# Optimization experiments

Hardware: AMD Instinct MI355X
Metric: run time of the kernel (lower is better)

## Reference

```python
import jax, jax.numpy as jnp
import numpy as np

NH, NKV, HD, H = 32, 8, 128, 4096
G = NH // NKV  # GQA group size = 4
EPS = 1e-5
SCALE = HD ** -0.5


def rms_norm(x, w, eps=EPS):
    # per-head RMSNorm over last dim, computed in fp32
    xf = x.astype(jnp.float32)
    var = jnp.mean(xf * xf, axis=-1, keepdims=True)
    return (w * (xf * jax.lax.rsqrt(var + eps)).astype(x.dtype))


def setup_inputs() -> dict:
    key = jax.random.key(0)
    ks = jax.random.split(key, 4)
    B, SQ, SKV = 4, 1024, 1601
    return {
        "hidden_states": jax.random.normal(ks[0], (B, SQ, H), jnp.float32),
        "cross_attention_states": jax.random.normal(ks[1], (B, SKV, H), jnp.float32),
        "wqkv": jax.random.normal(ks[2], ((NH + 2 * NKV) * HD, H), jnp.float32) * 0.02,
        "wo": jax.random.normal(ks[3], (NH * HD, H), jnp.float32) * 0.02,
        "q_norm_weight": jnp.ones((HD,), jnp.float32),
        "k_norm_weight": jnp.ones((HD,), jnp.float32),
    }


def reference(hidden_states, cross_attention_states, wqkv, wo, q_norm_weight, k_norm_weight):
    B, SQ, _ = hidden_states.shape
    SKV = cross_attention_states.shape[1]
    q_sz, kv_sz = NH * HD, NKV * HD

    # fused QKV projection on decoder tokens -> keep only q
    qkv_dec = jnp.einsum('bsh,oh->bso', hidden_states, wqkv)
    q = qkv_dec[..., :q_sz]
    # fused QKV projection on encoder tokens -> keep only k, v
    qkv_enc = jnp.einsum('bsh,oh->bso', cross_attention_states, wqkv)
    k = qkv_enc[..., q_sz:q_sz + kv_sz]
    v = qkv_enc[..., q_sz + kv_sz:]

    q = rms_norm(q.reshape(B, SQ, NH, HD), q_norm_weight)      # [B,SQ,NH,HD]
    k = rms_norm(k.reshape(B, SKV, NKV, HD), k_norm_weight)    # [B,SKV,NKV,HD]
    v = v.reshape(B, SKV, NKV, HD)

    # GQA: group query heads per kv head
    qg = q.reshape(B, SQ, NKV, G, HD)
    scores = jnp.einsum('bqkgd,bskd->bkgqs', qg, k) * SCALE    # [B,NKV,G,SQ,SKV]
    probs = jax.nn.softmax(scores, axis=-1)
    out = jnp.einsum('bkgqs,bskd->bqkgd', probs, v)            # [B,SQ,NKV,G,HD]
    out = out.reshape(B, SQ, NH * HD)
    return jnp.einsum('bso,ho->bsh', out, wo.T.T) if False else jnp.einsum('bsf,hf->bsh', out, wo)
```

## Files before the change

kernel.cpp:

```cpp
#include <hip/hip_runtime.h>
#include <cstdint>
#include <math.h>

typedef _Float16 f16;
typedef __attribute__((ext_vector_type(4))) _Float16 f16x4;
typedef __attribute__((ext_vector_type(8))) _Float16 f16x8;
typedef __attribute__((ext_vector_type(4))) float f32x4;

__device__ inline void gload_lds16(const void* g, void* l) {
  auto gp = reinterpret_cast<const __attribute__((address_space(1))) uint32_t*>(
      reinterpret_cast<uintptr_t>(g));
  auto lp = reinterpret_cast<__attribute__((address_space(3))) uint32_t*>(
      reinterpret_cast<uintptr_t>(l));
  __builtin_amdgcn_global_load_lds(gp, lp, 16 , 0, 0);
}

__global__ __launch_bounds__(256) void cvtzero_kernel(const float* __restrict__ s0, f16* __restrict__ d0,
                                                      const float* __restrict__ s1, f16* __restrict__ d1,
                                                      const float* __restrict__ s2, f16* __restrict__ d2,
                                                      float4* __restrict__ z) {
  int idx = blockIdx.x * blockDim.x + threadIdx.x;
  int stride = gridDim.x * blockDim.x;
  for (int i = idx; i < 18747392; i += stride) {
    const float* src; f16* dst; int k;
    if (i < 4194304) { src = s0; dst = d0; k = i; }
    else if (i < 10752000) { src = s1; dst = d1; k = i - 4194304; }
    else if (i < 17043456) { src = s2; dst = d2; k = i - 10752000; }
    else { float4 zr = {0.f, 0.f, 0.f, 0.f}; z[i - 17043456] = zr; continue; }
    float4 v = reinterpret_cast<const float4*>(src)[k];
    f16x4 h;
    h.x = (f16)v.x; h.y = (f16)v.y; h.z = (f16)v.z; h.w = (f16)v.w;
    reinterpret_cast<f16x4*>(dst)[k] = h;
  }
}

__global__ __launch_bounds__(256) void cvt_kernel(const float* __restrict__ src,
                                                  f16* __restrict__ dst, int n4) {
  int idx = blockIdx.x * blockDim.x + threadIdx.x;
  int stride = gridDim.x * blockDim.x;
  for (int i = idx; i < n4; i += stride) {
    float4 v = reinterpret_cast<const float4*>(src)[i];
    f16x4 h;
    h.x = (f16)v.x; h.y = (f16)v.y; h.z = (f16)v.z; h.w = (f16)v.w;
    reinterpret_cast<f16x4*>(dst)[i] = h;
  }
}

template <bool MB, int EPI>
__global__ __launch_bounds__(512, 2) void gemm256(const f16* __restrict__ A,
                                                  const f16* __restrict__ Bw,
                                                  float* __restrict__ C,
                                                  f16* __restrict__ Ch,
                                                  const float* __restrict__ wvec,
                                                  f16* __restrict__ Vtf,
                                                  int M, int N, int K) {
  __shared__ f16 As[2][256][64];
  __shared__ f16 Bs[2][256][64];
  const int tid = threadIdx.x;
  const int l = tid & 63, w = tid >> 6;
  const int lq = l & 15, lk = l >> 4;
  const int wm = w >> 2, wn = w & 3;
  const int nwg = gridDim.x * gridDim.y;
  const int p = blockIdx.y * gridDim.x + blockIdx.x;
  const int L = (p & 7) * (nwg >> 3) + (p >> 3);
  const int bx = L % gridDim.x, by = L / gridDim.x;
  const int brow = by * 256, bcol = bx * 256;
  const int KT = K >> 6;

  const int srow8 = w * 8 + (l >> 3);
  const int scol  = ((l & 7) ^ (l >> 3)) * 8;
  const int swz   = (lq & 7) << 4;

  f32x4 acc[8][4];
  f32x4 zf = {0.f, 0.f, 0.f, 0.f};
#pragma unroll
  for (int m = 0; m < 8; ++m)
#pragma unroll
    for (int n = 0; n < 4; ++n) acc[m][n] = zf;

  auto stageA = [&](int kt, int buf, int i) {
    int ra = brow + i * 64 + srow8;
    if (MB) ra = (ra < M) ? ra : (M - 1);
    gload_lds16(A + (size_t)ra * K + kt * 64 + scol,
                (char*)(&As[buf][0][0]) + i * 8192 + w * 1024);
  };
  auto stageB = [&](int kt, int buf, int i) {
    int rb = bcol + i * 64 + srow8;
    gload_lds16(Bw + (size_t)rb * K + kt * 64 + scol,
                (char*)(&Bs[buf][0][0]) + i * 8192 + w * 1024);
  };
  auto ldA = [&](int buf, int m, int kk) -> f16x8 {
    int r = wm * 128 + m * 16 + lq;
    return *reinterpret_cast<const f16x8*>(
        (char*)(&As[buf][0][0]) + r * 128 + ((kk * 64 + lk * 16) ^ swz));
  };
  auto ldB = [&](int buf, int n, int kk) -> f16x8 {
    int r = wn * 64 + n * 16 + lq;
    return *reinterpret_cast<const f16x8*>(
        (char*)(&Bs[buf][0][0]) + r * 128 + ((kk * 64 + lk * 16) ^ swz));
  };

#pragma unroll
  for (int i = 0; i < 4; ++i) stageA(0, 0, i);
#pragma unroll
  for (int i = 0; i < 4; ++i) stageB(0, 0, i);

  f16x8 avA[4][2], avB[4][2], bvA[2][2], bvB[2][2];
  for (int t = 0; t < KT; ++t) {
    const int buf = t & 1, nbuf = buf ^ 1;
    const bool pf = (t + 1 < KT);

    if (pf) {
      stageA(t + 1, nbuf, 0); stageA(t + 1, nbuf, 1);
      asm volatile("s_waitcnt vmcnt(2)" ::: "memory");
    } else {
      asm volatile("s_waitcnt vmcnt(0)" ::: "memory");
    }
    __builtin_amdgcn_s_barrier();

#pragma unroll
    for (int mm = 0; mm < 4; ++mm)
#pragma unroll
      for (int kk = 0; kk < 2; ++kk) avA[mm][kk] = ldA(buf, mm, kk);
#pragma unroll
    for (int nn = 0; nn < 2; ++nn)
#pragma unroll
      for (int kk = 0; kk < 2; ++kk) bvA[nn][kk] = ldB(buf, nn, kk);
    __builtin_amdgcn_s_setprio(1);
#pragma unroll
    for (int mm = 0; mm < 4; ++mm)
#pragma unroll
      for (int nn = 0; nn < 2; ++nn)
#pragma unroll
        for (int kk = 0; kk < 2; ++kk)
          acc[mm][nn] = __builtin_amdgcn_mfma_f32_16x16x32_f16(avA[mm][kk], bvA[nn][kk], acc[mm][nn], 0, 0, 0);
    __builtin_amdgcn_s_setprio(0);
#pragma unroll
    for (int mm = 0; mm < 4; ++mm)
#pragma unroll
      for (int kk = 0; kk < 2; ++kk) avB[mm][kk] = ldA(buf, 4 + mm, kk);
    if (pf) { stageA(t + 1, nbuf, 2); stageA(t + 1, nbuf, 3); }
    asm volatile("" ::: "memory");
    __builtin_amdgcn_s_barrier();

    __builtin_amdgcn_s_setprio(1);
#pragma unroll
    for (int mm = 0; mm < 4; ++mm)
#pragma unroll
      for (int nn = 0; nn < 2; ++nn)
#pragma unroll
        for (int kk = 0; kk < 2; ++kk)
          acc[4 + mm][nn] = __builtin_amdgcn_mfma_f32_16x16x32_f16(avB[mm][kk], bvA[nn][kk], acc[4 + mm][nn], 0, 0, 0);
    __builtin_amdgcn_s_setprio(0);
#pragma unroll
    for (int nn = 0; nn < 2; ++nn)
#pragma unroll
      for (int kk = 0; kk < 2; ++kk) bvB[nn][kk] = ldB(buf, 2 + nn, kk);
    if (pf) { stageB(t + 1, nbuf, 0); stageB(t + 1, nbuf, 1); }
    asm volatile("" ::: "memory");
    __builtin_amdgcn_s_barrier();

    __builtin_amdgcn_s_setprio(1);
#pragma unroll
    for (int mm = 0; mm < 4; ++mm)
#pragma unroll
      for (int nn = 0; nn < 2; ++nn)
#pragma unroll
        for (int kk = 0; kk < 2; ++kk)
          acc[4 + mm][2 + nn] = __builtin_amdgcn_mfma_f32_16x16x32_f16(avB[mm][kk], bvB[nn][kk], acc[4 + mm][2 + nn], 0, 0, 0);
    __builtin_amdgcn_s_setprio(0);
#pragma unroll
    for (int mm = 0; mm < 4; ++mm)
#pragma unroll
      for (int kk = 0; kk < 2; ++kk) avA[mm][kk] = ldA(buf, mm, kk);
    if (pf) { stageB(t + 1, nbuf, 2); stageB(t + 1, nbuf, 3); }
    asm volatile("" ::: "memory");
    __builtin_amdgcn_s_barrier();

    __builtin_amdgcn_s_setprio(1);
#pragma unroll
    for (int mm = 0; mm < 4; ++mm)
#pragma unroll
      for (int nn = 0; nn < 2; ++nn)
#pragma unroll
        for (int kk = 0; kk < 2; ++kk)
          acc[mm][2 + nn] = __builtin_amdgcn_mfma_f32_16x16x32_f16(avA[mm][kk], bvB[nn][kk], acc[mm][2 + nn], 0, 0, 0);
    __builtin_amdgcn_s_setprio(0);
  }

  if (EPI == 0) {
#pragma unroll
    for (int m = 0; m < 8; ++m) {
#pragma unroll
      for (int j = 0; j < 4; ++j) {
        int row = brow + wm * 128 + m * 16 + lk * 4 + j;
        if (MB && row >= M) continue;
        float* dst = C + (size_t)row * N + bcol + wn * 64 + lq;
#pragma unroll
        for (int n = 0; n < 4; ++n) dst[n * 16] = acc[m][n][j];
      }
    }
  } else if (EPI == 1) {
    __shared__ float ssq[256][4];
#pragma unroll
    for (int m = 0; m < 8; ++m)
#pragma unroll
      for (int j = 0; j < 4; ++j) {
        int lr = wm * 128 + m * 16 + lk * 4 + j;
        float pp = 0.f;
#pragma unroll
        for (int n = 0; n < 4; ++n) pp += acc[m][n][j] * acc[m][n][j];
        pp += __shfl_xor(pp, 1);
        pp += __shfl_xor(pp, 2);
        pp += __shfl_xor(pp, 4);
        pp += __shfl_xor(pp, 8);
        if (lq == 0) ssq[lr][wn] = pp;
      }
    asm volatile("" ::: "memory");
    __builtin_amdgcn_s_barrier();
    const int hh = wn >> 1;
    float wv[4];
#pragma unroll
    for (int n = 0; n < 4; ++n) wv[n] = wvec[(wn * 64 + n * 16 + lq) & 127];
#pragma unroll
    for (int m = 0; m < 8; ++m)
#pragma unroll
      for (int j = 0; j < 4; ++j) {
        int lr = wm * 128 + m * 16 + lk * 4 + j;
        float ss = ssq[lr][hh * 2] + ssq[lr][hh * 2 + 1];
        float rs = rsqrtf(ss * (1.0f / 128.0f) + 1e-5f) *
                   (0.08838834764831845f * 1.4426950408889634f);
        f16* dst = Ch + (size_t)(brow + lr) * N + bcol + wn * 64 + lq;
#pragma unroll
        for (int n = 0; n < 4; ++n) dst[n * 16] = (f16)(acc[m][n][j] * rs * wv[n]);
      }
  } else {
    const bool isK = (bcol < 1024);
    __shared__ float ssq[256][4];
    if (isK) {
#pragma unroll
      for (int m = 0; m < 8; ++m)
#pragma unroll
        for (int j = 0; j < 4; ++j) {
          int lr = wm * 128 + m * 16 + lk * 4 + j;
          float pp = 0.f;
#pragma unroll
          for (int n = 0; n < 4; ++n) pp += acc[m][n][j] * acc[m][n][j];
          pp += __shfl_xor(pp, 1);
          pp += __shfl_xor(pp, 2);
          pp += __shfl_xor(pp, 4);
          pp += __shfl_xor(pp, 8);
          if (lq == 0) ssq[lr][wn] = pp;
        }
      asm volatile("" ::: "memory");
      __builtin_amdgcn_s_barrier();
    }
    const int hh = wn >> 1;
    float wv[4];
    if (isK) {
#pragma unroll
      for (int n = 0; n < 4; ++n) wv[n] = wvec[(wn * 64 + n * 16 + lq) & 127];
    }
#pragma unroll
    for (int m = 0; m < 8; ++m) {
#pragma unroll
      for (int j = 0; j < 4; ++j) {
        int lr = wm * 128 + m * 16 + lk * 4 + j;
        int r = brow + lr;
        if (r >= M) continue;
        unsigned bb = (unsigned)r / 1601u;
        unsigned s = (unsigned)r - bb * 1601u;
        if (isK) {
          float ss = ssq[lr][hh * 2] + ssq[lr][hh * 2 + 1];
          float rs = rsqrtf(ss * (1.0f / 128.0f) + 1e-5f);
#pragma unroll
          for (int n = 0; n < 4; ++n) {
            int col = wn * 64 + n * 16 + lq;
            int kvh = (bcol + col) >> 7;
            int d = col & 127;
            Ch[((size_t)(bb * 8 + kvh) * 1664 + s) * 128 + d] =
                (f16)(acc[m][n][j] * rs * wv[n]);
          }
        } else {
#pragma unroll
          for (int n = 0; n < 4; ++n) {
            int col = bcol - 1024 + wn * 64 + n * 16 + lq;
            int kvh = col >> 7;
            int d = col & 127;
            Vtf[((size_t)(bb * 8 + kvh) * 128 + d) * 1664 + s] = (f16)acc[m][n][j];
          }
        }
      }
    }
  }
}

__global__ __launch_bounds__(256, 2) void attn_kernel(const f16* __restrict__ Qf,
                                                      const f16* __restrict__ Kf,
                                                      const f16* __restrict__ Vtf,
                                                      f16* __restrict__ Oa) {
  __shared__ f16 Ksm[2][64][128];
  __shared__ f16 Vsm[2][128][64];
  __shared__ f16 Psm[4][32][64];
  const int p = blockIdx.x;
  const int L = (p & 7) * 128 + (p >> 3);
  const int qt = L & 7, h = (L >> 3) & 31, b = L >> 8;
  const int kvh = h >> 2;
  const int tid = threadIdx.x;
  const int l = tid & 63, w = tid >> 6;
  const int lq = l & 15, lk = l >> 4;

  f16x8 qreg[2][4];
  const f16* Qbase = Qf + ((size_t)(b * 1024 + qt * 128 + w * 32)) * 4096 + h * 128;
#pragma unroll
  for (int qm = 0; qm < 2; ++qm)
#pragma unroll
    for (int ks = 0; ks < 4; ++ks)
      qreg[qm][ks] = *reinterpret_cast<const f16x8*>(
          Qbase + (size_t)(qm * 16 + lq) * 4096 + ks * 32 + lk * 8);

  const f16* Kb = Kf + (size_t)(b * 8 + kvh) * (1664 * 128);
  const f16* Vb = Vtf + (size_t)(b * 8 + kvh) * (128 * 1664);

  f32x4 o[2][8];
  f32x4 zf = {0.f, 0.f, 0.f, 0.f};
  f32x4 neg8 = {-8.f, -8.f, -8.f, -8.f};
#pragma unroll
  for (int qm = 0; qm < 2; ++qm)
#pragma unroll
    for (int dn = 0; dn < 8; ++dn) o[qm][dn] = zf;
  float lrow[2][4];
#pragma unroll
  for (int qm = 0; qm < 2; ++qm)
#pragma unroll
    for (int j = 0; j < 4; ++j) lrow[qm][j] = 0.f;

  char* Pw = (char*)(&Psm[w][0][0]);
  const int swzR = (lq & 7) << 4;

  auto stageK = [&](int t, int buf) {
#pragma unroll
    for (int i = 0; i < 4; ++i) {
      int row = w * 16 + i * 4 + lk;
      int cb = (lq * 16) ^ ((row & 7) << 4);
      gload_lds16(Kb + (size_t)(t * 64 + row) * 128 + (cb >> 1),
                  (char*)(&Ksm[buf][0][0]) + w * 4096 + i * 1024);
    }
  };
  auto stageV = [&](int t, int buf) {
#pragma unroll
    for (int i = 0; i < 4; ++i) {
      int r = w * 32 + i * 8 + (l >> 3);
      int cb = ((l & 7) * 16) ^ ((r & 7) << 4);
      gload_lds16(Vb + (size_t)r * 1664 + t * 64 + (cb >> 1),
                  (char*)(&Vsm[buf][0][0]) + w * 4096 + i * 1024);
    }
  };

  stageK(0, 0);
  stageV(0, 0);
  int cur = 0;
  for (int t = 0; t < 26; ++t) {
    if (t < 25) {
      stageK(t + 1, cur ^ 1);
      stageV(t + 1, cur ^ 1);
      asm volatile("s_waitcnt vmcnt(8)" ::: "memory");
    } else {
      asm volatile("s_waitcnt vmcnt(0)" ::: "memory");
    }
    __builtin_amdgcn_s_barrier();

    f32x4 s[2][4];
#pragma unroll
    for (int qm = 0; qm < 2; ++qm)
#pragma unroll
      for (int kn = 0; kn < 4; ++kn) s[qm][kn] = neg8;
    __builtin_amdgcn_s_setprio(1);
#pragma unroll
    for (int ks = 0; ks < 4; ++ks) {
      f16x8 bf[4];
#pragma unroll
      for (int kn = 0; kn < 4; ++kn)
        bf[kn] = *reinterpret_cast<const f16x8*>(
            (char*)(&Ksm[cur][0][0]) + (kn * 16 + lq) * 256 + ((ks * 64 + lk * 16) ^ swzR));
#pragma unroll
      for (int qm = 0; qm < 2; ++qm)
#pragma unroll
        for (int kn = 0; kn < 4; ++kn)
          s[qm][kn] = __builtin_amdgcn_mfma_f32_16x16x32_f16(qreg[qm][ks], bf[kn], s[qm][kn], 0, 0, 0);
    }
    __builtin_amdgcn_s_setprio(0);

    if (t == 25) {
#pragma unroll
      for (int kn = 0; kn < 4; ++kn) {
        bool valid = (kn * 16 + lq) < 1;
#pragma unroll
        for (int qm = 0; qm < 2; ++qm)
#pragma unroll
          for (int j = 0; j < 4; ++j) s[qm][kn][j] = valid ? s[qm][kn][j] : -1e30f;
      }
    }

#pragma unroll
    for (int qm = 0; qm < 2; ++qm) {
#pragma unroll
      for (int j = 0; j < 4; ++j) {
        float rsum = 0.f;
#pragma unroll
        for (int kn = 0; kn < 4; ++kn) {
          float pv = exp2f(s[qm][kn][j]);
          s[qm][kn][j] = pv;
          rsum += pv;
        }
        lrow[qm][j] += rsum;
        int prow = qm * 16 + lk * 4 + j;
        int swzW = lk << 5;
#pragma unroll
        for (int kn = 0; kn < 4; ++kn)
          *reinterpret_cast<f16*>(Pw + prow * 128 + (((kn * 16 + lq) * 2) ^ swzW)) =
              (f16)s[qm][kn][j];
      }
    }

    __builtin_amdgcn_s_setprio(1);
#pragma unroll
    for (int c = 0; c < 2; ++c) {
      f16x8 pa[2];
#pragma unroll
      for (int qm = 0; qm < 2; ++qm) {
        int prow = qm * 16 + lq;
        pa[qm] = *reinterpret_cast<const f16x8*>(
            Pw + prow * 128 + ((c * 64 + lk * 16) ^ (((lq >> 2) & 3) << 5)));
      }
      f16x8 vb[8];
#pragma unroll
      for (int dn = 0; dn < 8; ++dn)
        vb[dn] = *reinterpret_cast<const f16x8*>(
            (char*)(&Vsm[cur][0][0]) + (dn * 16 + lq) * 128 + ((c * 64 + lk * 16) ^ swzR));
#pragma unroll
      for (int qm = 0; qm < 2; ++qm)
#pragma unroll
        for (int dn = 0; dn < 8; ++dn)
          o[qm][dn] = __builtin_amdgcn_mfma_f32_16x16x32_f16(pa[qm], vb[dn], o[qm][dn], 0, 0, 0);
    }
    __builtin_amdgcn_s_setprio(0);
    __builtin_amdgcn_s_barrier();
    cur ^= 1;
  }

#pragma unroll
  for (int qm = 0; qm < 2; ++qm) {
#pragma unroll
    for (int j = 0; j < 4; ++j) {
      float fl = lrow[qm][j];
      fl += __shfl_xor(fl, 1);
      fl += __shfl_xor(fl, 2);
      fl += __shfl_xor(fl, 4);
      fl += __shfl_xor(fl, 8);
      float il = 1.0f / fl;
      int token = b * 1024 + qt * 128 + w * 32 + qm * 16 + lk * 4 + j;
      f16* dst = Oa + (size_t)token * 4096 + h * 128;
#pragma unroll
      for (int dn = 0; dn < 8; ++dn) dst[dn * 16 + lq] = (f16)(o[qm][dn][j] * il);
    }
  }
}

extern "C" void kernel_launch(void* const* d_in, const int* in_sizes, int n_in,
                              void* d_out, int out_size, void* d_ws, size_t ws_size,
                              hipStream_t stream) {
  const float* hidden = (const float*)d_in[0];
  const float* cross  = (const float*)d_in[1];
  const float* wqkv   = (const float*)d_in[2];
  const float* wo     = (const float*)d_in[3];
  const float* qw     = (const float*)d_in[4];
  const float* kw     = (const float*)d_in[5];

  char* ws = (char*)d_ws;
  f16* hidden_h = (f16*)(ws + 0);
  f16* attn_h   = hidden_h;
  f16* wqkv_h = (f16*)(ws + 33554432);
  f16* cross_h = (f16*)(ws + 83886080);
  f16* wo_h    = (f16*)(ws + 83886080);
  f16* k_h  = (f16*)(ws + 136347648);
  f16* vt_h = (f16*)(ws + 136347648 + 13631488);
  f16* q_h = (f16*)d_out;

  cvtzero_kernel<<<2048, 256, 0, stream>>>(hidden, hidden_h, cross, cross_h,
                                           wqkv, wqkv_h, (float4*)(ws + 136347648));
  gemm256<true, 2><<<dim3(8, 26), 512, 0, stream>>>(
      cross_h, wqkv_h + (size_t)4096 * 4096, nullptr, k_h, kw, vt_h, 6404, 2048, 4096);
  cvt_kernel<<<2048, 256, 0, stream>>>(wo, wo_h, 16777216 / 4);
  gemm256<false, 1><<<dim3(16, 16), 512, 0, stream>>>(
      hidden_h, wqkv_h, nullptr, q_h, qw, nullptr, 4096, 4096, 4096);
  attn_kernel<<<1024, 256, 0, stream>>>(q_h, k_h, vt_h, attn_h);
  gemm256<false, 0><<<dim3(16, 16), 512, 0, stream>>>(
      attn_h, wo_h, (float*)d_out, nullptr, nullptr, nullptr, 4096, 4096, 4096);
}
```

Before: 605.7 us.

## Single-buffer attention K/V tiles for occupancy and fuse wo conversion into cvtzero

The attention kernel drops double-buffered K/V LDS tiles and uses single buffers. The next K tile is loaded after the QK step and the next V tile after the PV step, with launch bounds raised to allow three blocks per CU. This trades explicit prefetch overlap for more resident waves and adds extra waits and barriers per iteration. Separately, the wo fp32->fp16 conversion moves into the combined cvtzero kernel when the workspace is large enough, saving one launch but making the first kernel longer.

Result: slower. 675.0 us (+11.4%).

```diff
diff --git a/kernel.cpp b/kernel.cpp
--- a/kernel.cpp
+++ b/kernel.cpp
@@ -18,15 +18,20 @@
 __global__ __launch_bounds__(256) void cvtzero_kernel(const float* __restrict__ s0, f16* __restrict__ d0,
                                                       const float* __restrict__ s1, f16* __restrict__ d1,
                                                       const float* __restrict__ s2, f16* __restrict__ d2,
+                                                      const float* __restrict__ s3, f16* __restrict__ d3,
+                                                      int nwo,
                                                       float4* __restrict__ z) {
   int idx = blockIdx.x * blockDim.x + threadIdx.x;
   int stride = gridDim.x * blockDim.x;
-  for (int i = idx; i < 18747392; i += stride) {
+  const int nz0 = 17043456 + nwo;
+  const int total = nz0 + 1703936;
+  for (int i = idx; i < total; i += stride) {
     const float* src; f16* dst; int k;
     if (i < 4194304) { src = s0; dst = d0; k = i; }
     else if (i < 10752000) { src = s1; dst = d1; k = i - 4194304; }
     else if (i < 17043456) { src = s2; dst = d2; k = i - 10752000; }
-    else { float4 zr = {0.f, 0.f, 0.f, 0.f}; z[i - 17043456] = zr; continue; }
+    else if (i < nz0) { src = s3; dst = d3; k = i - 17043456; }
+    else { float4 zr = {0.f, 0.f, 0.f, 0.f}; z[i - nz0] = zr; continue; }
     float4 v = reinterpret_cast<const float4*>(src)[k];
     f16x4 h;
     h.x = (f16)v.x; h.y = (f16)v.y; h.z = (f16)v.z; h.w = (f16)v.w;
@@ -295,12 +300,12 @@
   }
 }
 
-__global__ __launch_bounds__(256, 2) void attn_kernel(const f16* __restrict__ Qf,
+__global__ __launch_bounds__(256, 3) void attn_kernel(const f16* __restrict__ Qf,
                                                       const f16* __restrict__ Kf,
                                                       const f16* __restrict__ Vtf,
                                                       f16* __restrict__ Oa) {
-  __shared__ f16 Ksm[2][64][128];
-  __shared__ f16 Vsm[2][128][64];
+  __shared__ f16 Ksm[64][128];
+  __shared__ f16 Vsm[128][64];
   __shared__ f16 Psm[4][32][64];
   const int p = blockIdx.x;
   const int L = (p & 7) * 128 + (p >> 3);
@@ -338,38 +343,31 @@
   char* Pw = (char*)(&Psm[w][0][0]);
   const int swzR = (lq & 7) << 4;
 
-  auto stageK = [&](int t, int buf) {
+  auto stageK = [&](int t) {
 #pragma unroll
     for (int i = 0; i < 4; ++i) {
       int row = w * 16 + i * 4 + lk;
       int cb = (lq * 16) ^ ((row & 7) << 4);
       gload_lds16(Kb + (size_t)(t * 64 + row) * 128 + (cb >> 1),
-                  (char*)(&Ksm[buf][0][0]) + w * 4096 + i * 1024);
+                  (char*)(&Ksm[0][0]) + w * 4096 + i * 1024);
     }
   };
-  auto stageV = [&](int t, int buf) {
+  auto stageV = [&](int t) {
 #pragma unroll
     for (int i = 0; i < 4; ++i) {
       int r = w * 32 + i * 8 + (l >> 3);
       int cb = ((l & 7) * 16) ^ ((r & 7) << 4);
       gload_lds16(Vb + (size_t)r * 1664 + t * 64 + (cb >> 1),
-                  (char*)(&Vsm[buf][0][0]) + w * 4096 + i * 1024);
+                  (char*)(&Vsm[0][0]) + w * 4096 + i * 1024);
     }
   };
 
-  stageK(0, 0);
-  stageV(0, 0);
-  int cur = 0;
+  stageK(0);
+  stageV(0);
+  asm volatile("s_waitcnt vmcnt(0)" ::: "memory");
+  __builtin_amdgcn_s_barrier();
+
   for (int t = 0; t < 26; ++t) {
-    if (t < 25) {
-      stageK(t + 1, cur ^ 1);
-      stageV(t + 1, cur ^ 1);
-      asm volatile("s_waitcnt vmcnt(8)" ::: "memory");
-    } else {
-      asm volatile("s_waitcnt vmcnt(0)" ::: "memory");
-    }
-    __builtin_amdgcn_s_barrier();
-
     f32x4 s[2][4];
 #pragma unroll
     for (int qm = 0; qm < 2; ++qm)
@@ -382,7 +380,7 @@
 #pragma unroll
       for (int kn = 0; kn < 4; ++kn)
         bf[kn] = *reinterpret_cast<const f16x8*>(
-            (char*)(&Ksm[cur][0][0]) + (kn * 16 + lq) * 256 + ((ks * 64 + lk * 16) ^ swzR));
+            (char*)(&Ksm[0][0]) + (kn * 16 + lq) * 256 + ((ks * 64 + lk * 16) ^ swzR));
 #pragma unroll
       for (int qm = 0; qm < 2; ++qm)
 #pragma unroll
@@ -390,6 +388,10 @@
           s[qm][kn] = __builtin_amdgcn_mfma_f32_16x16x32_f16(qreg[qm][ks], bf[kn], s[qm][kn], 0, 0, 0);
     }
     __builtin_amdgcn_s_setprio(0);
+
+    asm volatile("s_waitcnt vmcnt(0)" ::: "memory");
+    __builtin_amdgcn_s_barrier();
+    if (t < 25) stageK(t + 1);
 
     if (t == 25) {
 #pragma unroll
@@ -437,7 +439,7 @@
 #pragma unroll
       for (int dn = 0; dn < 8; ++dn)
         vb[dn] = *reinterpret_cast<const f16x8*>(
-            (char*)(&Vsm[cur][0][0]) + (dn * 16 + lq) * 128 + ((c * 64 + lk * 16) ^ swzR));
+            (char*)(&Vsm[0][0]) + (dn * 16 + lq) * 128 + ((c * 64 + lk * 16) ^ swzR));
 #pragma unroll
       for (int qm = 0; qm < 2; ++qm)
 #pragma unroll
@@ -445,8 +447,10 @@
           o[qm][dn] = __builtin_amdgcn_mfma_f32_16x16x32_f16(pa[qm], vb[dn], o[qm][dn], 0, 0, 0);
     }
     __builtin_amdgcn_s_setprio(0);
-    __builtin_amdgcn_s_barrier();
-    cur ^= 1;
+
+    asm volatile("s_waitcnt vmcnt(0)" ::: "memory");
+    __builtin_amdgcn_s_barrier();
+    if (t < 25) stageV(t + 1);
   }
 
 #pragma unroll
@@ -482,16 +486,21 @@
   f16* attn_h   = hidden_h;
   f16* wqkv_h = (f16*)(ws + 33554432);
   f16* cross_h = (f16*)(ws + 83886080);
-  f16* wo_h    = (f16*)(ws + 83886080);
   f16* k_h  = (f16*)(ws + 136347648);
   f16* vt_h = (f16*)(ws + 136347648 + 13631488);
   f16* q_h = (f16*)d_out;
 
+  const bool fuse_wo = (ws_size >= (size_t)197165056);
+  f16* wo_h = fuse_wo ? (f16*)(ws + 163610624) : (f16*)(ws + 83886080);
+
   cvtzero_kernel<<<2048, 256, 0, stream>>>(hidden, hidden_h, cross, cross_h,
-                                           wqkv, wqkv_h, (float4*)(ws + 136347648));
+                                           wqkv, wqkv_h, wo, wo_h,
+                                           fuse_wo ? 4194304 : 0,
+                                           (float4*)(ws + 136347648));
   gemm256<true, 2><<<dim3(8, 26), 512, 0, stream>>>(
       cross_h, wqkv_h + (size_t)4096 * 4096, nullptr, k_h, kw, vt_h, 6404, 2048, 4096);
-  cvt_kernel<<<2048, 256, 0, stream>>>(wo, wo_h, 16777216 / 4);
+  if (!fuse_wo)
+    cvt_kernel<<<2048, 256, 0, stream>>>(wo, wo_h, 16777216 / 4);
   gemm256<false, 1><<<dim3(16, 16), 512, 0, stream>>>(
       hidden_h, wqkv_h, nullptr, q_h, qw, nullptr, 4096, 4096, 4096);
   attn_kernel<<<1024, 256, 0, stream>>>(q_h, k_h, vt_h, attn_h);
```
